# Kernel tuning notes

Hardware: AMD Instinct MI355X
Metric: run time of the kernel (lower is better)

The kernel has to match this reference:

```python
import jax, jax.numpy as jnp
import numpy as np

B, N_CLS, M_TIME, U_LAB = 1024, 96, 256, 40


def setup_inputs() -> dict:
    key = jax.random.key(0)
    k1, k2, k3 = jax.random.split(key, 3)
    logits = jax.random.normal(k1, (B, N_CLS, M_TIME), dtype=jnp.float32)
    # module treats inputs as per-timestep class probabilities (softmax output of CRNN)
    out_padded = jax.nn.softmax(logits, axis=1)
    label = jax.random.randint(k2, (B, U_LAB), 1, N_CLS, dtype=jnp.int32)  # 0 is blank
    unpadded_w = jax.random.randint(k3, (B,), 512, 4 * M_TIME + 1, dtype=jnp.int32)
    return {"out_padded": out_padded, "label": label, "unpadded_w": unpadded_w}


def _alpha(probs, lab, T, L):
    # probs: (M, N) time-major class probabilities; lab: (U,) label indices; T traced int.
    # Faithful to compute_alpha: per-timestep renormalization over [start, end),
    # recurrence computed for s in [start, L).
    M = probs.shape[0]
    s_idx = jnp.arange(L)
    i_idx = jnp.maximum((s_idx - 1) // 2, 0)
    is_odd = (s_idx % 2) == 1
    cls = jnp.where(is_odd, lab[i_idx], 0)  # blank = class 0 for even s
    # skip (a[t-1][s-2]) allowed only for odd s != 1 with non-repeated label
    skip = is_odd & (s_idx != 1) & (lab[i_idx] != lab[jnp.maximum(i_idx - 1, 0)])

    p0 = probs[0]
    row0 = jnp.zeros((L,), probs.dtype).at[0].set(p0[0]).at[1].set(p0[lab[0]])
    c0 = row0[0] + row0[1]
    row0 = jnp.where((s_idx < 2) & (c0 > 0), row0 / jnp.where(c0 > 0, c0, 1.0), row0)

    def step(prev, t):
        start = jnp.maximum(0, L - 2 * (T - t))
        end = jnp.minimum(2 * t + 2, L)
        pm1 = jnp.concatenate([jnp.zeros((1,), prev.dtype), prev[:-1]])
        pm2 = jnp.concatenate([jnp.zeros((2,), prev.dtype), prev[:-2]])
        val = (prev
               + jnp.where(s_idx > 0, pm1, 0.0)
               + jnp.where(skip, pm2, 0.0)) * probs[t, cls]
        val = jnp.where(s_idx >= start, val, 0.0)  # s < start stays zero
        nmask = (s_idx >= start) & (s_idx < end)
        c = jnp.sum(jnp.where(nmask, val, 0.0))
        val = jnp.where(nmask & (c > 0), val / jnp.where(c > 0, c, 1.0), val)
        return val, val

    _, rows = jax.lax.scan(step, row0, jnp.arange(1, M))
    a = jnp.concatenate([row0[None, :], rows], axis=0)  # (M, L)
    return jnp.where((jnp.arange(M) < T)[:, None], a, 0.0)  # rows >= T are zero


def _ctc_single(out_cw, lab, w):
    probs = out_cw.T  # (M, N): time x classes, as in torch.transpose(out, 1, 0)
    M = probs.shape[0]
    U = lab.shape[0]
    L = 2 * U + 1
    T = w // 4
    a = _alpha(probs, lab, T, L)
    # 'beta' faithful to source: alpha on CLASS-flipped probs (torch.fliplr on (T,N))
    # with reversed labels, then flipud+fliplr of the (T,L) result.
    b_raw = _alpha(probs[:, ::-1], lab[::-1], T, L)
    src = T - 1 - jnp.arange(M)
    valid = (src >= 0) & (src < M)
    b = jnp.where(valid[:, None], b_raw[jnp.clip(src, 0, M - 1)], 0.0)[:, ::-1]
    ab = a * b  # (M, L)
    s_idx = jnp.arange(L)
    cls = jnp.where((s_idx % 2) == 1, lab[jnp.maximum((s_idx - 1) // 2, 0)], 0)
    lh = jnp.sum(ab / probs[:, cls], axis=1)  # (M,)
    tmask = jnp.arange(M) < T
    return -jnp.sum(jnp.where(tmask, jnp.log(jnp.where(tmask, lh, 1.0)), 0.0))


def reference(out_padded, label, unpadded_w):
    losses = jax.vmap(_ctc_single)(out_padded, label, unpadded_w)  # (B,)
    return jnp.sum(losses)
```

## Files before the change

kernel.cpp:

```cpp
#include <hip/hip_runtime.h>
#include <cmath>

namespace {
constexpr int BN = 1024;
constexpr int NC = 96;
constexpr int MT = 256;
constexpr int UL = 40;
constexpr int LS = 81;
constexpr int PAIRS = 41;

template <int CTRL>
__device__ __forceinline__ float dppf(float v) {
  return __builtin_bit_cast(
      float, __builtin_amdgcn_update_dpp(0, __builtin_bit_cast(int, v), CTRL,
                                         0xf, 0xf, true));
}
__device__ __forceinline__ float rl63(float x) {
  return __builtin_bit_cast(
      float, __builtin_amdgcn_readlane(__builtin_bit_cast(int, x), 63));
}
__device__ __forceinline__ float wave_sum(float x) {
  x += dppf<0x111>(x);
  x += dppf<0x112>(x);
  x += dppf<0x114>(x);
  x += dppf<0x118>(x);
  x += dppf<0x142>(x);
  x += dppf<0x143>(x);
  return rl63(x);
}
__device__ __forceinline__ float wave_shr1(float v) { return dppf<0x138>(v); }
__device__ __forceinline__ float fast_rcp(float x) {
  return __builtin_amdgcn_rcpf(x);
}
__device__ __forceinline__ unsigned packu(float a, float b) {
  unsigned ua = __builtin_bit_cast(unsigned, a) >> 16;
  unsigned ub = __builtin_bit_cast(unsigned, b) & 0xffff0000u;
  return ua | ub;
}
__device__ __forceinline__ float bf_lo(unsigned u) {
  return __builtin_bit_cast(float, u << 16);
}
__device__ __forceinline__ float bf_hi(unsigned u) {
  return __builtin_bit_cast(float, u & 0xffff0000u);
}

constexpr float FQ = 1e8f;
constexpr float SEPS = 1e-30f;

__global__ __launch_bounds__(64) void chain_kernel(
    const float* __restrict__ gout, const int* __restrict__ glabel,
    const int* __restrict__ gw, unsigned* __restrict__ xa,
    unsigned* __restrict__ xb) {
  const int bx = blockIdx.x;
  const int b = bx >> 1, ph = bx & 1;
  const int i = threadIdx.x;
  const float* P = gout + (size_t)b * (NC * MT);
  const int* lab = glabel + b * UL;
  const int T = gw[b] >> 2;

  const int s0 = 2 * i, s1 = s0 + 1;
  const float h0f = (i <= 40) ? 1.f : 0.f;
  const float h1f = (i <= 39) ? 1.f : 0.f;
  const int iw = (i <= 40) ? i : 40;
  const bool act = (i <= 40);

  const float* pB;
  const float* pL;
  float mskf;
  unsigned* outp;
  if (ph == 0) {
    const int li = (i < UL) ? lab[i] : 0;
    const int lm = (i >= 1 && i < UL) ? lab[i - 1] : 0;
    pB = P;
    pL = P + (size_t)li * MT;
    mskf = (i >= 1 && i <= 39 && li != lm) ? 1.f : 0.f;
    outp = xa + ((size_t)b * PAIRS + iw) * MT;
  } else {
    const int rli = (i < UL) ? lab[UL - 1 - i] : 0;
    const int rlm = (i >= 1 && i < UL) ? lab[UL - i] : 0;
    pB = P + (size_t)(NC - 1) * MT;
    pL = P + (size_t)(NC - 1 - rli) * MT;
    mskf = (i >= 1 && i <= 39 && rli != rlm) ? 1.f : 0.f;
    outp = xb + ((size_t)b * PAIRS + (40 - iw)) * MT;
  }

  float pbv[8], plv[8];
  float4 LA = *(const float4*)(pB + 0), LB = *(const float4*)(pB + 4);
  float4 MA = *(const float4*)(pL + 0), MB = *(const float4*)(pL + 4);
  pbv[0] = LA.x; pbv[1] = LA.y; pbv[2] = LA.z; pbv[3] = LA.w;
  pbv[4] = LB.x; pbv[5] = LB.y; pbv[6] = LB.z; pbv[7] = LB.w;
  plv[0] = MA.x; plv[1] = MA.y; plv[2] = MA.z; plv[3] = MA.w;
  plv[4] = MB.x; plv[5] = MB.y; plv[6] = MB.z; plv[7] = MB.w;
  LA = *(const float4*)(pB + 8); LB = *(const float4*)(pB + 12);
  MA = *(const float4*)(pL + 8); MB = *(const float4*)(pL + 12);

  float v0 = (i == 0) ? pbv[0] : 0.f;
  float v1 = (i == 0) ? plv[0] : 0.f;
  float ss = wave_sum(v0 + v1);
  float r0q = FQ * fast_rcp(fmaxf(ss, SEPS));
  float r1q = FQ * fast_rcp(fmaxf(ss * r0q, SEPS));
  float r2q = FQ * fast_rcp(fmaxf(ss * r0q * r1q, SEPS));

  float f0[8], f1[8], fs[8];
  fs[0] = ss;
  if (ph == 0) {
    f0[0] = (i == 0) ? 1.f : 0.f;
    f1[0] = f0[0];
  } else {
    f0[0] = v0;
    f1[0] = 0.f;
  }

#define CTC_STEP(T_, K_)                                              \
  {                                                                   \
    float pm1 = wave_shr1(v1);                                        \
    if (ph == 1 && (K_) >= 1) f1[(K_)-1] = pm1;                       \
    const float rh0 = r0q * h0f, rh1 = r0q * h1f;                     \
    float u0 = v0 + pm1;                                              \
    float u1 = (v0 + v1) + pm1 * mskf;                                \
    const int start_ = LS - 2 * (T - (T_));                           \
    if (s0 < start_) u0 = 0.f;                                        \
    if (s1 < start_) u1 = 0.f;                                        \
    const float x0 = u0 * rh0, x1 = u1 * rh1;                         \
    float n0 = x0 * pbv[(K_)];                                        \
    float n1 = x1 * plv[(K_)];                                        \
    float ssn = wave_sum(n0 + n1);                                    \
    float rn = FQ * fast_rcp(fmaxf(ssn, SEPS) * r1q * r2q);           \
    rn = fminf(fmaxf(rn, 1e-20f), 1e20f);                             \
    r0q = r1q; r1q = r2q; r2q = rn;                                   \
    v0 = n0; v1 = n1;                                                 \
    fs[(K_)] = ssn;                                                   \
    if (ph == 0) { f0[(K_)] = x0; f1[(K_)] = x1; }                    \
    else { f0[(K_)] = n0; }                                           \
  }

#define CTC_BURST(T0_)                                                \
  {                                                                   \
    if (ph == 1) f1[7] = wave_shr1(v1);                               \
    if (act) {                                                        \
      unsigned ob[8];                                                 \
      _Pragma("unroll")                                               \
      for (int k = 0; k < 8; ++k) {                                   \
        float inv = fast_rcp(fmaxf(fs[k], SEPS));                     \
        ob[k] = packu(f0[k] * inv, f1[k] * inv);                      \
      }                                                               \
      if ((T0_) + 7 < T) {                                            \
        *reinterpret_cast<uint4*>(outp + (T0_)) =                     \
            make_uint4(ob[0], ob[1], ob[2], ob[3]);                   \
        *reinterpret_cast<uint4*>(outp + (T0_) + 4) =                 \
            make_uint4(ob[4], ob[5], ob[6], ob[7]);                   \
      } else {                                                        \
        _Pragma("unroll")                                             \
        for (int k = 0; k < 8; ++k)                                   \
          if ((T0_) + k < T) outp[(T0_) + k] = ob[k];                 \
      }                                                               \
    }                                                                 \
  }

#pragma unroll
  for (int k = 1; k < 8; ++k) CTC_STEP(k, k);
  CTC_BURST(0);

  for (int t0 = 8; t0 < T; t0 += 8) {
    pbv[0] = LA.x; pbv[1] = LA.y; pbv[2] = LA.z; pbv[3] = LA.w;
    pbv[4] = LB.x; pbv[5] = LB.y; pbv[6] = LB.z; pbv[7] = LB.w;
    plv[0] = MA.x; plv[1] = MA.y; plv[2] = MA.z; plv[3] = MA.w;
    plv[4] = MB.x; plv[5] = MB.y; plv[6] = MB.z; plv[7] = MB.w;
    int np = t0 + 8;
    if (np > 248) np = 248;
    LA = *(const float4*)(pB + np); LB = *(const float4*)(pB + np + 4);
    MA = *(const float4*)(pL + np); MB = *(const float4*)(pL + np + 4);
#pragma unroll
    for (int k = 0; k < 8; ++k) CTC_STEP(t0 + k, k);
    CTC_BURST(t0);
  }
#undef CTC_STEP
#undef CTC_BURST
}

__global__ __launch_bounds__(256) void combine_kernel(
    const int* __restrict__ gw, const unsigned* __restrict__ xa,
    const unsigned* __restrict__ xb, float* __restrict__ loss_out) {
  const int b = blockIdx.x;
  const int tid = threadIdx.x;
  const int T = gw[b] >> 2;
  float lsum = 0.f;
  if (tid < T) {
    const unsigned* A = xa + (size_t)b * PAIRS * MT + tid;
    const unsigned* Bb = xb + (size_t)b * PAIRS * MT + (T - 1 - tid);
    float d = 0.f;
#pragma unroll
    for (int p = 0; p < PAIRS; ++p) {
      const unsigned av = A[p * MT];
      const unsigned bv = Bb[p * MT];
      d = fmaf(bf_lo(av), bf_lo(bv), d);
      d = fmaf(bf_hi(av), bf_hi(bv), d);
    }
    lsum = -__logf(fmaxf(d, 1e-37f));
  }
  lsum = wave_sum(lsum);
  __shared__ float part[4];
  if ((tid & 63) == 0) part[tid >> 6] = lsum;
  __syncthreads();
  if (tid == 0) {
    float L = part[0] + part[1] + part[2] + part[3];
    loss_out[b] = fminf(fmaxf(L, -1e30f), 1e30f);
  }
}

__global__ void reduce_kernel(const float* __restrict__ loss_in,
                              float* __restrict__ out) {
  __shared__ double sm[256];
  const int tid = threadIdx.x;
  double s = 0.0;
  for (int k = tid; k < BN; k += 256) s += (double)loss_in[k];
  sm[tid] = s;
  __syncthreads();
  for (int w = 128; w >= 1; w >>= 1) {
    if (tid < w) sm[tid] += sm[tid + w];
    __syncthreads();
  }
  if (tid == 0) out[0] = (float)sm[0];
}
}

extern "C" void kernel_launch(void* const* d_in, const int* in_sizes, int n_in,
                              void* d_out, int out_size, void* d_ws, size_t ws_size,
                              hipStream_t stream) {
  const float* gout = (const float*)d_in[0];
  const int* glabel = (const int*)d_in[1];
  const int* gw = (const int*)d_in[2];
  unsigned* xa = (unsigned*)d_ws;
  unsigned* xb = xa + (size_t)BN * PAIRS * MT;
  float* loss = (float*)(xb + (size_t)BN * PAIRS * MT);
  chain_kernel<<<2 * BN, 64, 0, stream>>>(gout, glabel, gw, xa, xb);
  combine_kernel<<<BN, 256, 0, stream>>>(gw, xa, xb, loss);
  reduce_kernel<<<1, 256, 0, stream>>>(loss, (float*)d_out);
}
```

Measured before the change: 202.6 us.

## Fuse alpha/beta chains and combine into one block using shared-memory rows

Runs the forward and reversed chains as two waves of one block per sample and exchanges the first half of normalized rows through shared memory instead of global workspace. Each wave computes the per-timestep likelihood terms once the partner's matching row is available, so the separate combine kernel and the global round trip of packed bf16 rows go away. In exchange, block-wide barriers are added inside the time loop during the second half, and there is about 42KB of LDS per block.

Result: slower. 219.1 us (+8.1%).

```diff
diff --git a/kernel.cpp b/kernel.cpp
--- a/kernel.cpp
+++ b/kernel.cpp
@@ -8,6 +8,7 @@
 constexpr int UL = 40;
 constexpr int LS = 81;
 constexpr int PAIRS = 41;
+constexpr int ROWS = 128;
 
 template <int CTRL>
 __device__ __forceinline__ float dppf(float v) {
@@ -47,13 +48,14 @@
 constexpr float FQ = 1e8f;
 constexpr float SEPS = 1e-30f;
 
-__global__ __launch_bounds__(64) void chain_kernel(
+__global__ __launch_bounds__(128) void ctc_fused_kernel(
     const float* __restrict__ gout, const int* __restrict__ glabel,
-    const int* __restrict__ gw, unsigned* __restrict__ xa,
-    unsigned* __restrict__ xb) {
-  const int bx = blockIdx.x;
-  const int b = bx >> 1, ph = bx & 1;
-  const int i = threadIdx.x;
+    const int* __restrict__ gw, float* __restrict__ loss_out) {
+  __shared__ unsigned srows[2][ROWS * PAIRS];
+  __shared__ float spart[2];
+  const int b = blockIdx.x;
+  const int ph = threadIdx.x >> 6;
+  const int i = threadIdx.x & 63;
   const float* P = gout + (size_t)b * (NC * MT);
   const int* lab = glabel + b * UL;
   const int T = gw[b] >> 2;
@@ -67,22 +69,24 @@
   const float* pB;
   const float* pL;
   float mskf;
-  unsigned* outp;
+  int col;
   if (ph == 0) {
     const int li = (i < UL) ? lab[i] : 0;
     const int lm = (i >= 1 && i < UL) ? lab[i - 1] : 0;
     pB = P;
     pL = P + (size_t)li * MT;
     mskf = (i >= 1 && i <= 39 && li != lm) ? 1.f : 0.f;
-    outp = xa + ((size_t)b * PAIRS + iw) * MT;
+    col = iw;
   } else {
     const int rli = (i < UL) ? lab[UL - 1 - i] : 0;
     const int rlm = (i >= 1 && i < UL) ? lab[UL - i] : 0;
     pB = P + (size_t)(NC - 1) * MT;
     pL = P + (size_t)(NC - 1 - rli) * MT;
     mskf = (i >= 1 && i <= 39 && rli != rlm) ? 1.f : 0.f;
-    outp = xb + ((size_t)b * PAIRS + (40 - iw)) * MT;
-  }
+    col = 40 - iw;
+  }
+  unsigned* mrow = srows[ph];
+  const unsigned* orow = srows[1 - ph];
 
   float pbv[8], plv[8];
   float4 LA = *(const float4*)(pB + 0), LB = *(const float4*)(pB + 4);
@@ -110,6 +114,7 @@
     f0[0] = v0;
     f1[0] = 0.f;
   }
+  float acc = 0.f;
 
 #define CTC_STEP(T_, K_)                                              \
   {                                                                   \
@@ -134,32 +139,45 @@
     else { f0[(K_)] = n0; }                                           \
   }
 
-#define CTC_BURST(T0_)                                                \
+#define CTC_PUB(T0_)                                                  \
   {                                                                   \
     if (ph == 1) f1[7] = wave_shr1(v1);                               \
-    if (act) {                                                        \
-      unsigned ob[8];                                                 \
+    if (act && (T0_) < ROWS) {                                        \
       _Pragma("unroll")                                               \
       for (int k = 0; k < 8; ++k) {                                   \
         float inv = fast_rcp(fmaxf(fs[k], SEPS));                     \
-        ob[k] = packu(f0[k] * inv, f1[k] * inv);                      \
-      }                                                               \
-      if ((T0_) + 7 < T) {                                            \
-        *reinterpret_cast<uint4*>(outp + (T0_)) =                     \
-            make_uint4(ob[0], ob[1], ob[2], ob[3]);                   \
-        *reinterpret_cast<uint4*>(outp + (T0_) + 4) =                 \
-            make_uint4(ob[4], ob[5], ob[6], ob[7]);                   \
-      } else {                                                        \
-        _Pragma("unroll")                                             \
-        for (int k = 0; k < 8; ++k)                                   \
-          if ((T0_) + k < T) outp[(T0_) + k] = ob[k];                 \
+        mrow[((T0_) + k) * PAIRS + col] =                             \
+            packu(f0[k] * inv, f1[k] * inv);                          \
       }                                                               \
     }                                                                 \
   }
 
+#define CTC_TERMS(T0_)                                                \
+  if (2 * (T0_) >= T - 15) {                                          \
+    __syncthreads();                                                  \
+    _Pragma("unroll")                                                 \
+    for (int kk = 0; kk < 8; ++kk) {                                  \
+      const int k = (T0_) + kk;                                       \
+      if (k < T) {                                                    \
+        const int tb = T - 1 - k;                                     \
+        const bool ck = (k + (T0_) >= T - 8);                         \
+        const bool mine =                                             \
+            (ph == 0) ? ck : (ck && (tb + (tb & ~7) < T - 8));        \
+        if (mine) {                                                   \
+          const unsigned av = orow[tb * PAIRS + col];                 \
+          const float inv = fast_rcp(fmaxf(fs[kk], SEPS));            \
+          const float pr =                                            \
+              (bf_lo(av) * f0[kk] + bf_hi(av) * f1[kk]) * inv;        \
+          const float d = wave_sum(pr);                               \
+          acc += __logf(fmaxf(d, 1e-37f));                            \
+        }                                                             \
+      }                                                               \
+    }                                                                 \
+  }
+
 #pragma unroll
   for (int k = 1; k < 8; ++k) CTC_STEP(k, k);
-  CTC_BURST(0);
+  CTC_PUB(0);
 
   for (int t0 = 8; t0 < T; t0 += 8) {
     pbv[0] = LA.x; pbv[1] = LA.y; pbv[2] = LA.z; pbv[3] = LA.w;
@@ -172,38 +190,17 @@
     MA = *(const float4*)(pL + np); MB = *(const float4*)(pL + np + 4);
 #pragma unroll
     for (int k = 0; k < 8; ++k) CTC_STEP(t0 + k, k);
-    CTC_BURST(t0);
+    CTC_PUB(t0);
+    CTC_TERMS(t0);
   }
 #undef CTC_STEP
-#undef CTC_BURST
-}
-
-__global__ __launch_bounds__(256) void combine_kernel(
-    const int* __restrict__ gw, const unsigned* __restrict__ xa,
-    const unsigned* __restrict__ xb, float* __restrict__ loss_out) {
-  const int b = blockIdx.x;
-  const int tid = threadIdx.x;
-  const int T = gw[b] >> 2;
-  float lsum = 0.f;
-  if (tid < T) {
-    const unsigned* A = xa + (size_t)b * PAIRS * MT + tid;
-    const unsigned* Bb = xb + (size_t)b * PAIRS * MT + (T - 1 - tid);
-    float d = 0.f;
-#pragma unroll
-    for (int p = 0; p < PAIRS; ++p) {
-      const unsigned av = A[p * MT];
-      const unsigned bv = Bb[p * MT];
-      d = fmaf(bf_lo(av), bf_lo(bv), d);
-      d = fmaf(bf_hi(av), bf_hi(bv), d);
-    }
-    lsum = -__logf(fmaxf(d, 1e-37f));
-  }
-  lsum = wave_sum(lsum);
-  __shared__ float part[4];
-  if ((tid & 63) == 0) part[tid >> 6] = lsum;
+#undef CTC_PUB
+#undef CTC_TERMS
+
+  if (i == 0) spart[ph] = -acc;
   __syncthreads();
-  if (tid == 0) {
-    float L = part[0] + part[1] + part[2] + part[3];
+  if (threadIdx.x == 0) {
+    float L = spart[0] + spart[1];
     loss_out[b] = fminf(fmaxf(L, -1e30f), 1e30f);
   }
 }
@@ -230,10 +227,7 @@
   const float* gout = (const float*)d_in[0];
   const int* glabel = (const int*)d_in[1];
   const int* gw = (const int*)d_in[2];
-  unsigned* xa = (unsigned*)d_ws;
-  unsigned* xb = xa + (size_t)BN * PAIRS * MT;
-  float* loss = (float*)(xb + (size_t)BN * PAIRS * MT);
-  chain_kernel<<<2 * BN, 64, 0, stream>>>(gout, glabel, gw, xa, xb);
-  combine_kernel<<<BN, 256, 0, stream>>>(gw, xa, xb, loss);
+  float* loss = (float*)d_ws;
+  ctc_fused_kernel<<<BN, 128, 0, stream>>>(gout, glabel, gw, loss);
   reduce_kernel<<<1, 256, 0, stream>>>(loss, (float*)d_out);
 }
```

## Batch wave reductions per 8-step burst and renormalize once per burst

Applied to the files above, without the earlier changes.

Removes the per-timestep wave_sum and reciprocal from the serial recurrence. Each step now only stores its local partial sum, and the eight sums are reduced together at the end of the burst with interleaved DPP levels. The state is renormalized once per burst using the last step's sum. The start-masking is also dropped for the early timesteps where it cannot apply (t0+47<T). This shortens the latency-bound dependency chain, at the cost of letting values drift in scale across up to eight unnormalized steps, which risks underflow or overflow.

New measurement: 206.7 us. +2.0%, slower.

```diff
diff --git a/kernel.cpp b/kernel.cpp
--- a/kernel.cpp
+++ b/kernel.cpp
@@ -96,52 +96,60 @@
 
   float v0 = (i == 0) ? pbv[0] : 0.f;
   float v1 = (i == 0) ? plv[0] : 0.f;
-  float ss = wave_sum(v0 + v1);
-  float r0q = FQ * fast_rcp(fmaxf(ss, SEPS));
-  float r1q = FQ * fast_rcp(fmaxf(ss * r0q, SEPS));
-  float r2q = FQ * fast_rcp(fmaxf(ss * r0q * r1q, SEPS));
-
-  float f0[8], f1[8], fs[8];
-  fs[0] = ss;
+
+  float f0[8], f1[8], sv[8];
   if (ph == 0) {
+    sv[0] = v0 + v1;
     f0[0] = (i == 0) ? 1.f : 0.f;
     f1[0] = f0[0];
+    v0 *= FQ;
+    v1 *= FQ;
   } else {
+    v0 *= FQ;
+    v1 *= FQ;
+    sv[0] = v0 + v1;
     f0[0] = v0;
     f1[0] = 0.f;
   }
 
-#define CTC_STEP(T_, K_)                                              \
+#define CTC_STEP(T_, K_, DOMASK)                                      \
   {                                                                   \
     float pm1 = wave_shr1(v1);                                        \
     if (ph == 1 && (K_) >= 1) f1[(K_)-1] = pm1;                       \
-    const float rh0 = r0q * h0f, rh1 = r0q * h1f;                     \
     float u0 = v0 + pm1;                                              \
     float u1 = (v0 + v1) + pm1 * mskf;                                \
-    const int start_ = LS - 2 * (T - (T_));                           \
-    if (s0 < start_) u0 = 0.f;                                        \
-    if (s1 < start_) u1 = 0.f;                                        \
-    const float x0 = u0 * rh0, x1 = u1 * rh1;                         \
+    if (DOMASK) {                                                     \
+      const int start_ = LS - 2 * (T - (T_));                         \
+      if (s0 < start_) u0 = 0.f;                                      \
+      if (s1 < start_) u1 = 0.f;                                      \
+    }                                                                 \
+    const float x0 = u0 * h0f, x1 = u1 * h1f;                         \
     float n0 = x0 * pbv[(K_)];                                        \
     float n1 = x1 * plv[(K_)];                                        \
-    float ssn = wave_sum(n0 + n1);                                    \
-    float rn = FQ * fast_rcp(fmaxf(ssn, SEPS) * r1q * r2q);           \
-    rn = fminf(fmaxf(rn, 1e-20f), 1e20f);                             \
-    r0q = r1q; r1q = r2q; r2q = rn;                                   \
+    sv[(K_)] = n0 + n1;                                               \
     v0 = n0; v1 = n1;                                                 \
-    fs[(K_)] = ssn;                                                   \
     if (ph == 0) { f0[(K_)] = x0; f1[(K_)] = x1; }                    \
     else { f0[(K_)] = n0; }                                           \
   }
 
+#define WS_LEVEL(CTRL)                                                \
+  {                                                                   \
+    _Pragma("unroll")                                                 \
+    for (int k = 0; k < 8; ++k) sv[k] += dppf<CTRL>(sv[k]);           \
+  }
+
 #define CTC_BURST(T0_)                                                \
   {                                                                   \
-    if (ph == 1) f1[7] = wave_shr1(v1);                               \
+    if (ph == 1) f1[7] = wave_shr1(v1);          \
+    WS_LEVEL(0x111) WS_LEVEL(0x112) WS_LEVEL(0x114)                   \
+    WS_LEVEL(0x118) WS_LEVEL(0x142) WS_LEVEL(0x143)                   \
+    _Pragma("unroll")                                                 \
+    for (int k = 0; k < 8; ++k) sv[k] = rl63(sv[k]);                  \
     if (act) {                                                        \
       unsigned ob[8];                                                 \
       _Pragma("unroll")                                               \
       for (int k = 0; k < 8; ++k) {                                   \
-        float inv = fast_rcp(fmaxf(fs[k], SEPS));                     \
+        float inv = fast_rcp(fmaxf(sv[k], SEPS));                     \
         ob[k] = packu(f0[k] * inv, f1[k] * inv);                      \
       }                                                               \
       if ((T0_) + 7 < T) {                                            \
@@ -155,27 +163,44 @@
           if ((T0_) + k < T) outp[(T0_) + k] = ob[k];                 \
       }                                                               \
     }                                                                 \
-  }
-
-#pragma unroll
-  for (int k = 1; k < 8; ++k) CTC_STEP(k, k);
+    float rb = FQ * fast_rcp(fmaxf(sv[7], SEPS));                     \
+    rb = fminf(fmaxf(rb, 1e-20f), 1e20f);                             \
+    v0 *= rb; v1 *= rb;                                               \
+  }
+
+#define CTC_UNPACK()                                                  \
+  {                                                                   \
+    pbv[0] = LA.x; pbv[1] = LA.y; pbv[2] = LA.z; pbv[3] = LA.w;       \
+    pbv[4] = LB.x; pbv[5] = LB.y; pbv[6] = LB.z; pbv[7] = LB.w;       \
+    plv[0] = MA.x; plv[1] = MA.y; plv[2] = MA.z; plv[3] = MA.w;       \
+    plv[4] = MB.x; plv[5] = MB.y; plv[6] = MB.z; plv[7] = MB.w;       \
+    int np = t0 + 8;                                                  \
+    if (np > 248) np = 248;                                           \
+    LA = *(const float4*)(pB + np); LB = *(const float4*)(pB + np + 4); \
+    MA = *(const float4*)(pL + np); MB = *(const float4*)(pL + np + 4); \
+  }
+
+#pragma unroll
+  for (int k = 1; k < 8; ++k) CTC_STEP(k, k, false);
   CTC_BURST(0);
 
-  for (int t0 = 8; t0 < T; t0 += 8) {
-    pbv[0] = LA.x; pbv[1] = LA.y; pbv[2] = LA.z; pbv[3] = LA.w;
-    pbv[4] = LB.x; pbv[5] = LB.y; pbv[6] = LB.z; pbv[7] = LB.w;
-    plv[0] = MA.x; plv[1] = MA.y; plv[2] = MA.z; plv[3] = MA.w;
-    plv[4] = MB.x; plv[5] = MB.y; plv[6] = MB.z; plv[7] = MB.w;
-    int np = t0 + 8;
-    if (np > 248) np = 248;
-    LA = *(const float4*)(pB + np); LB = *(const float4*)(pB + np + 4);
-    MA = *(const float4*)(pL + np); MB = *(const float4*)(pL + np + 4);
-#pragma unroll
-    for (int k = 0; k < 8; ++k) CTC_STEP(t0 + k, k);
+  int t0 = 8;
+  for (; t0 + 47 < T; t0 += 8) {
+    CTC_UNPACK();
+#pragma unroll
+    for (int k = 0; k < 8; ++k) CTC_STEP(t0 + k, k, false);
+    CTC_BURST(t0);
+  }
+  for (; t0 < T; t0 += 8) {
+    CTC_UNPACK();
+#pragma unroll
+    for (int k = 0; k < 8; ++k) CTC_STEP(t0 + k, k, true);
     CTC_BURST(t0);
   }
 #undef CTC_STEP
 #undef CTC_BURST
+#undef CTC_UNPACK
+#undef WS_LEVEL
 }
 
 __global__ __launch_bounds__(256) void combine_kernel(
```
